# Kernel optimization log

Measured on AMD Instinct MI355X. Metric: run time of the kernel, lower is better.

Reference implementation:

```python
import jax, jax.numpy as jnp
import numpy as np

B, P, K, H, C = 8, 4096, 20, 64, 40  # clouds, points/cloud, knn k, hidden_feat, num_classes
NEG = 0.2  # LeakyReLU negative slope used by the repo MLP


def setup_inputs() -> dict:
    key = jax.random.key(0)
    ks = jax.random.split(key, 16)
    w = lambda k, shape: (jax.random.normal(k, shape, jnp.float32) / np.sqrt(shape[0]))
    return {
        "x": jax.random.normal(ks[0], (B * P, 3), jnp.float32),
        "batch": jnp.repeat(jnp.arange(B, dtype=jnp.int32), P),
        "W1": w(ks[1], (2 * 3, H)), "b1": jnp.zeros((H,), jnp.float32),
        "W2": w(ks[2], (2 * H, H)), "b2": jnp.zeros((H,), jnp.float32),
        "W3": w(ks[3], (2 * H, H)), "b3": jnp.zeros((H,), jnp.float32),
        "Wl": w(ks[4], (3 * H, 1024)), "bl": jnp.zeros((1024,), jnp.float32),
        "Wm1": w(ks[5], (1024, 256)), "bm1": jnp.zeros((256,), jnp.float32),
        "Wm2": w(ks[6], (256, 128)), "bm2": jnp.zeros((128,), jnp.float32),
        "Wo": w(ks[7], (128, C)), "bo": jnp.zeros((C,), jnp.float32),
    }


def _knn_idx(x):
    # x: [B,P,d] -> indices of K nearest neighbors (excluding self): [B,P,K]
    d2 = jnp.sum(x * x, axis=-1)  # [B,P]
    dist = d2[:, :, None] + d2[:, None, :] - 2.0 * jnp.einsum('bpd,bqd->bpq', x, x)
    dist = dist + jnp.eye(x.shape[1], dtype=x.dtype) * 1e10  # mask self-loops
    return jax.lax.top_k(-dist, K)[1]


def _edge_conv(x, W, b):
    # DynamicEdgeConv with max aggregation: nn([x_i, x_j - x_i]) maxed over K neighbors
    idx = _knn_idx(x)                                    # [B,P,K]
    x_j = jax.vmap(lambda xb, ib: xb[ib])(x, idx)        # [B,P,K,d]
    x_i = jnp.broadcast_to(x[:, :, None, :], x_j.shape)  # [B,P,K,d]
    feat = jnp.concatenate([x_i, x_j - x_i], axis=-1)    # [B,P,K,2d]
    h = jax.nn.leaky_relu(feat @ W + b, NEG)             # [B,P,K,H]
    return jnp.max(h, axis=2)                            # [B,P,H]


def reference(x, batch, W1, b1, W2, b2, W3, b3, Wl, bl, Wm1, bm1, Wm2, bm2, Wo, bo):
    # batch is sorted with equal-size clouds -> reshape to [B,P,3]
    xb = x.reshape(B, P, 3)
    x1 = _edge_conv(xb, W1, b1)
    x2 = _edge_conv(x1, W2, b2)
    x3 = _edge_conv(x2, W3, b3)
    h = jnp.concatenate([x1, x2, x3], axis=-1)           # [B,P,3H]
    h = jax.nn.leaky_relu(h @ Wl + bl, NEG)
    h = jax.nn.leaky_relu(h @ Wm1 + bm1, NEG)            # dropout = identity (eval)
    h = jax.nn.leaky_relu(h @ Wm2 + bm2, NEG)
    out = h @ Wo + bo                                    # [B,P,C]
    return jax.nn.log_softmax(out, axis=-1).reshape(B * P, C)
```

## Files before the change

kernel.cpp:

```cpp
#include <hip/hip_runtime.h>
#include <cstddef>
#include <cstdint>

constexpr int B_ = 8, P_ = 4096, K_ = 20, H_ = 64, C_ = 40;
constexpr int NPT = B_ * P_;
#define NEG_SLOPE 0.2f

typedef unsigned long long u64;
typedef unsigned int u32;
typedef unsigned short u16;
typedef __attribute__((ext_vector_type(8))) short bf16x8;
typedef __attribute__((ext_vector_type(4))) float f32x4;

__device__ inline u16 f2bf(float v) {
    u32 bits = __float_as_uint(v);
    return (u16)((bits + 0x7FFFu + ((bits >> 16) & 1)) >> 16);
}
__device__ inline float bf2f(u16 h) { return __uint_as_float((u32)h << 16); }

__device__ __forceinline__ void bubble20f(float (&a)[K_], float key) {
    float carry = key;
#pragma unroll
    for (int s = 0; s < K_; ++s) {
        float as = a[s];
        a[s]  = fminf(carry, as);
        carry = fmaxf(carry, as);
    }
}
__device__ __forceinline__ float mkkey(float dist, int cid) {
    return __uint_as_float((__float_as_uint(dist) & 0xFFFFF000u) | (u32)cid);
}

template <int D>
__global__ __launch_bounds__(256) void d2_kernel(const float* __restrict__ x,
                                                 float* __restrict__ d2) {
    int i = blockIdx.x * 256 + threadIdx.x;
    if (i >= NPT) return;
    const float* r = x + (size_t)i * D;
    float s = 0.f;
#pragma unroll
    for (int d = 0; d < D; ++d) { float v = r[d]; s += v * v; }
    d2[i] = s;
}

__global__ __launch_bounds__(256) void d2cvt3_kernel(const float* __restrict__ x,
                                                     float* __restrict__ d2,
                                                     u16* __restrict__ xh,
                                                     u16* __restrict__ xm,
                                                     u16* __restrict__ xl) {
    int i = blockIdx.x * 256 + threadIdx.x;
    if (i >= NPT) return;
    const float* r = x + (size_t)i * 64;
    float s = 0.f;
#pragma unroll
    for (int d8 = 0; d8 < 64; d8 += 8) {
        float4 v0 = *(const float4*)(r + d8);
        float4 v1 = *(const float4*)(r + d8 + 4);
        s += v0.x * v0.x + v0.y * v0.y + v0.z * v0.z + v0.w * v0.w;
        s += v1.x * v1.x + v1.y * v1.y + v1.z * v1.z + v1.w * v1.w;
        float av[8] = {v0.x, v0.y, v0.z, v0.w, v1.x, v1.y, v1.z, v1.w};
        bf16x8 vh, vm, vl;
#pragma unroll
        for (int j = 0; j < 8; ++j) {
            u16 h = f2bf(av[j]);
            float r1 = av[j] - bf2f(h);
            u16 m = f2bf(r1);
            float r2 = r1 - bf2f(m);
            vh[j] = (short)h; vm[j] = (short)m; vl[j] = (short)f2bf(r2);
        }
        *(bf16x8*)(xh + (size_t)i * 64 + d8) = vh;
        *(bf16x8*)(xm + (size_t)i * 64 + d8) = vm;
        *(bf16x8*)(xl + (size_t)i * 64 + d8) = vl;
    }
    d2[i] = s;
}

template <int D>
__global__ __launch_bounds__(256) void knnf_kernel(const float* __restrict__ x,
                                                   const float* __restrict__ d2,
                                                   int* __restrict__ idx) {
    __shared__ float sQT[D][68];
    __shared__ float sCT[D][68];
    __shared__ float sD[64][68];

    int b = blockIdx.y;
    int q0 = blockIdx.x * 64;
    const float* xc  = x + (size_t)b * P_ * D;
    const float* d2b = d2 + (size_t)b * P_;

    int t = threadIdx.x;
    int ty = t >> 4, tx = t & 15;
    int w = t >> 6, ln = t & 63;
    int qs = w * 16 + (ln >> 2);
    int cs = ln & 3;

    if (t < 64) {
#pragma unroll
        for (int d = 0; d < D; ++d) sQT[d][t] = xc[(size_t)(q0 + t) * D + d];
    }
    float qd2i[4];
#pragma unroll
    for (int i = 0; i < 4; ++i) qd2i[i] = d2b[q0 + ty * 4 + i];

    float a[K_];
#pragma unroll
    for (int s = 0; s < K_; ++s)
        a[s] = __uint_as_float(0x7F7FF000u | (u32)s);
    const float PINV = __uint_as_float(0x7F800000u);
    const float BIGF = __uint_as_float(0x7F7FFFFFu);

    float p0 = PINV, p1 = PINV, p2 = PINV, p3 = PINV;
    int pcnt = 0;
    float kthr = BIGF;

#pragma unroll 1
    for (int c0 = 0; c0 < P_; c0 += 64) {
        __syncthreads();
        if (t < 64) {
#pragma unroll
            for (int d = 0; d < D; ++d) sCT[d][t] = xc[(size_t)(c0 + t) * D + d];
        }
        __syncthreads();

        float acc[4][4] = {};
#pragma unroll
        for (int kk = 0; kk < D; ++kk) {
            float4 aq = *(const float4*)&sQT[kk][ty * 4];
            float4 bc = *(const float4*)&sCT[kk][tx * 4];
            acc[0][0] = fmaf(aq.x, bc.x, acc[0][0]); acc[0][1] = fmaf(aq.x, bc.y, acc[0][1]);
            acc[0][2] = fmaf(aq.x, bc.z, acc[0][2]); acc[0][3] = fmaf(aq.x, bc.w, acc[0][3]);
            acc[1][0] = fmaf(aq.y, bc.x, acc[1][0]); acc[1][1] = fmaf(aq.y, bc.y, acc[1][1]);
            acc[1][2] = fmaf(aq.y, bc.z, acc[1][2]); acc[1][3] = fmaf(aq.y, bc.w, acc[1][3]);
            acc[2][0] = fmaf(aq.z, bc.x, acc[2][0]); acc[2][1] = fmaf(aq.z, bc.y, acc[2][1]);
            acc[2][2] = fmaf(aq.z, bc.z, acc[2][2]); acc[2][3] = fmaf(aq.z, bc.w, acc[2][3]);
            acc[3][0] = fmaf(aq.w, bc.x, acc[3][0]); acc[3][1] = fmaf(aq.w, bc.y, acc[3][1]);
            acc[3][2] = fmaf(aq.w, bc.z, acc[3][2]); acc[3][3] = fmaf(aq.w, bc.w, acc[3][3]);
        }
        float cd2j[4];
#pragma unroll
        for (int j = 0; j < 4; ++j) cd2j[j] = d2b[c0 + tx * 4 + j];
        bool diag = (q0 == c0);
#pragma unroll
        for (int i = 0; i < 4; ++i) {
            float dd[4];
#pragma unroll
            for (int j = 0; j < 4; ++j) {
                float v = (qd2i[i] + cd2j[j]) - 2.f * acc[i][j];
                if (diag && (ty * 4 + i == tx * 4 + j)) v += 1e10f;
                dd[j] = fmaxf(v, 0.f);
            }
            *(float4*)&sD[ty * 4 + i][tx * 4] = make_float4(dd[0], dd[1], dd[2], dd[3]);
        }
        __syncthreads();

        float dvv[16];
        float mn = 3.4e38f;
#pragma unroll
        for (int u = 0; u < 16; ++u) {
            dvv[u] = sD[qs][cs + u * 4];
            mn = fminf(mn, dvv[u]);
        }
        if (__any(mn <= kthr)) {
#pragma unroll
            for (int u = 0; u < 16; ++u) {
                float dv = dvv[u];
                if (__any(dv <= kthr)) {
                    float key = mkkey(dv, c0 + cs + u * 4);
                    bool pass = key < a[K_ - 1];
                    p3 = pass ? p2 : p3;
                    p2 = pass ? p1 : p2;
                    p1 = pass ? p0 : p1;
                    p0 = pass ? key : p0;
                    pcnt = pass ? pcnt + 1 : pcnt;
                    if (__any(pcnt >= 4)) {
                        bubble20f(a, p3); bubble20f(a, p2); bubble20f(a, p1); bubble20f(a, p0);
                        p0 = p1 = p2 = p3 = PINV; pcnt = 0;
                        kthr = __uint_as_float(__float_as_uint(a[K_ - 1]) | 0xFFFu);
                    }
                }
            }
        }
    }
    bubble20f(a, p3); bubble20f(a, p2); bubble20f(a, p1); bubble20f(a, p0);

    int* op = idx + ((size_t)(b * P_ + q0 + qs)) * K_;
#pragma unroll 1
    for (int k = 0; k < K_; ++k) {
        float v = a[0];
        float v1 = __shfl_xor(v, 1);
        v = fminf(v, v1);
        float v2 = __shfl_xor(v, 2);
        v = fminf(v, v2);
        bool win = (__float_as_uint(a[0]) == __float_as_uint(v));
#pragma unroll
        for (int s = 0; s < K_ - 1; ++s) a[s] = win ? a[s + 1] : a[s];
        a[K_ - 1] = win ? BIGF : a[K_ - 1];
        if (cs == 0)
            op[k] = b * P_ + (int)(__float_as_uint(v) & 0xFFFu);
    }
}

__global__ __launch_bounds__(256) void knnm64_kernel(const u16* __restrict__ xh,
                                                     const u16* __restrict__ xm,
                                                     const u16* __restrict__ xl,
                                                     const float* __restrict__ d2,
                                                     int* __restrict__ idx) {
    __shared__ u16 sH[64 * 64];
    __shared__ u16 sM[64 * 64];
    __shared__ u16 sL[64 * 64];
    __shared__ float sd2[P_];

    int b = blockIdx.y;
    int q0 = blockIdx.x * 64;
    const u16* xhb = xh + (size_t)b * P_ * 64;
    const u16* xmb = xm + (size_t)b * P_ * 64;
    const u16* xlb = xl + (size_t)b * P_ * 64;
    const float* d2b = d2 + (size_t)b * P_;

    int t = threadIdx.x, w = t >> 6, ln = t & 63;
    int q  = ln & 15;
    int ss = ln >> 4;

    for (int i = t; i < P_ / 4; i += 256)
        ((float4*)sd2)[i] = ((const float4*)d2b)[i];

    int qrow = q0 + w * 16 + q;
    bf16x8 qh[2], qm[2], ql[2];
#pragma unroll
    for (int kt = 0; kt < 2; ++kt) {
        size_t off = (size_t)qrow * 64 + kt * 32 + ss * 8;
        qh[kt] = *(const bf16x8*)(xhb + off);
        qm[kt] = *(const bf16x8*)(xmb + off);
        ql[kt] = *(const bf16x8*)(xlb + off);
    }

    __syncthreads();
    float qd2 = sd2[qrow];

    float a[K_];
#pragma unroll
    for (int s = 0; s < K_; ++s)
        a[s] = __uint_as_float(0x7F7FF000u | (u32)s);
    const float PINV = __uint_as_float(0x7F800000u);
    const float BIGF = __uint_as_float(0x7F7FFFFFu);

    float p0 = PINV, p1 = PINV, p2 = PINV, p3 = PINV;
    int pcnt = 0;
    float kthr = BIGF;

    int sr = t >> 2;
    int sk2 = (t & 3) * 32;
    int sbase = sr * 128, sswz = (sr & 7) << 4;
    size_t sgof = (size_t)sr * 64 + (t & 3) * 16;

#pragma unroll 1
    for (int c0 = 0; c0 < P_; c0 += 64) {
        __syncthreads();
        {
            size_t g = (size_t)c0 * 64 + sgof;
            bf16x8 h0 = *(const bf16x8*)(xhb + g);
            bf16x8 h1 = *(const bf16x8*)(xhb + g + 8);
            bf16x8 m0 = *(const bf16x8*)(xmb + g);
            bf16x8 m1 = *(const bf16x8*)(xmb + g + 8);
            bf16x8 l0 = *(const bf16x8*)(xlb + g);
            bf16x8 l1 = *(const bf16x8*)(xlb + g + 8);
            *(bf16x8*)((char*)sH + sbase + (sk2 ^ sswz)) = h0;
            *(bf16x8*)((char*)sH + sbase + ((sk2 + 16) ^ sswz)) = h1;
            *(bf16x8*)((char*)sM + sbase + (sk2 ^ sswz)) = m0;
            *(bf16x8*)((char*)sM + sbase + ((sk2 + 16) ^ sswz)) = m1;
            *(bf16x8*)((char*)sL + sbase + (sk2 ^ sswz)) = l0;
            *(bf16x8*)((char*)sL + sbase + ((sk2 + 16) ^ sswz)) = l1;
        }
        __syncthreads();

        f32x4 acc[4];
#pragma unroll
        for (int nt = 0; nt < 4; ++nt) {
            acc[nt] = (f32x4){0.f, 0.f, 0.f, 0.f};
            int r = nt * 16 + q;
            int base = r * 128, swz = (r & 7) << 4;
#pragma unroll
            for (int kt = 0; kt < 2; ++kt) {
                int k2 = kt * 64 + ss * 16;
                bf16x8 ch = *(const bf16x8*)((char*)sH + base + (k2 ^ swz));
                bf16x8 cm = *(const bf16x8*)((char*)sM + base + (k2 ^ swz));
                bf16x8 cl = *(const bf16x8*)((char*)sL + base + (k2 ^ swz));
                acc[nt] = __builtin_amdgcn_mfma_f32_16x16x32_bf16(cm, qm[kt], acc[nt], 0, 0, 0);
                acc[nt] = __builtin_amdgcn_mfma_f32_16x16x32_bf16(cl, qh[kt], acc[nt], 0, 0, 0);
                acc[nt] = __builtin_amdgcn_mfma_f32_16x16x32_bf16(ch, ql[kt], acc[nt], 0, 0, 0);
                acc[nt] = __builtin_amdgcn_mfma_f32_16x16x32_bf16(cm, qh[kt], acc[nt], 0, 0, 0);
                acc[nt] = __builtin_amdgcn_mfma_f32_16x16x32_bf16(ch, qm[kt], acc[nt], 0, 0, 0);
                acc[nt] = __builtin_amdgcn_mfma_f32_16x16x32_bf16(ch, qh[kt], acc[nt], 0, 0, 0);
            }
        }

        float dvv[4][4];
        float mn = 3.4e38f;
#pragma unroll
        for (int nt = 0; nt < 4; ++nt) {
#pragma unroll
            for (int r = 0; r < 4; ++r) {
                int cID = c0 + nt * 16 + ss * 4 + r;
                float dv = (qd2 + sd2[cID]) - 2.f * acc[nt][r];
                if (cID == qrow) dv += 1e10f;
                dv = fmaxf(dv, 0.f);
                dvv[nt][r] = dv;
                mn = fminf(mn, dv);
            }
        }
        if (__any(mn <= kthr)) {
#pragma unroll
            for (int nt = 0; nt < 4; ++nt) {
#pragma unroll
                for (int r = 0; r < 4; ++r) {
                    float dv = dvv[nt][r];
                    if (__any(dv <= kthr)) {
                        float key = mkkey(dv, c0 + nt * 16 + ss * 4 + r);
                        bool pass = key < a[K_ - 1];
                        p3 = pass ? p2 : p3;
                        p2 = pass ? p1 : p2;
                        p1 = pass ? p0 : p1;
                        p0 = pass ? key : p0;
                        pcnt = pass ? pcnt + 1 : pcnt;
                        if (__any(pcnt >= 4)) {
                            bubble20f(a, p3); bubble20f(a, p2); bubble20f(a, p1); bubble20f(a, p0);
                            p0 = p1 = p2 = p3 = PINV; pcnt = 0;
                            kthr = __uint_as_float(__float_as_uint(a[K_ - 1]) | 0xFFFu);
                        }
                    }
                }
            }
        }
    }
    bubble20f(a, p3); bubble20f(a, p2); bubble20f(a, p1); bubble20f(a, p0);

    int* op = idx + ((size_t)(b * P_ + qrow)) * K_;
#pragma unroll 1
    for (int k = 0; k < K_; ++k) {
        float v = a[0];
        float v1 = __shfl_xor(v, 16);
        v = fminf(v, v1);
        float v2 = __shfl_xor(v, 32);
        v = fminf(v, v2);
        bool win = (__float_as_uint(a[0]) == __float_as_uint(v));
#pragma unroll
        for (int s = 0; s < K_ - 1; ++s) a[s] = win ? a[s + 1] : a[s];
        a[K_ - 1] = win ? BIGF : a[K_ - 1];
        if (ss == 0)
            op[k] = b * P_ + (int)(__float_as_uint(v) & 0xFFFu);
    }
}

__global__ __launch_bounds__(256) void prep_kernel(const float* __restrict__ W2,
                                                   const float* __restrict__ b2,
                                                   const float* __restrict__ W3,
                                                   const float* __restrict__ b3,
                                                   const float* __restrict__ Wl,
                                                   const float* __restrict__ Wm1,
                                                   const float* __restrict__ Wm2,
                                                   float* __restrict__ Wpk2, float* __restrict__ bpk2,
                                                   float* __restrict__ Wpk3, float* __restrict__ bpk3,
                                                   u16* __restrict__ WlT,
                                                   u16* __restrict__ Wm1T,
                                                   u16* __restrict__ Wm2T) {
    int t = blockIdx.x * 256 + threadIdx.x;
    if (t < 8192) {
        int d = t >> 7, h2 = t & 127;
        Wpk2[t] = (h2 < 64) ? W2[d * 64 + h2] : W2[(64 + d) * 64 + (h2 - 64)];
        if (t < 128) bpk2[t] = (t < 64) ? b2[t] : 0.f;
    } else if (t < 16384) {
        int t2 = t - 8192;
        int d = t2 >> 7, h2 = t2 & 127;
        Wpk3[t2] = (h2 < 64) ? W3[d * 64 + h2] : W3[(64 + d) * 64 + (h2 - 64)];
        if (t2 < 128) bpk3[t2] = (t2 < 64) ? b3[t2] : 0.f;
    } else if (t < 212992) {
        int t2 = t - 16384;
        int k = t2 >> 10, n = t2 & 1023;
        WlT[(size_t)n * 192 + k] = f2bf(Wl[t2]);
    } else if (t < 475136) {
        int t2 = t - 212992;
        int k = t2 >> 8, n = t2 & 255;
        Wm1T[(size_t)n * 1024 + k] = f2bf(Wm1[t2]);
    } else if (t < 507904) {
        int t2 = t - 475136;
        int k = t2 >> 7, n = t2 & 127;
        Wm2T[(size_t)n * 256 + k] = f2bf(Wm2[t2]);
    }
}

__global__ __launch_bounds__(256) void uv3_kernel(const float* __restrict__ x,
                                                  const float* __restrict__ W,
                                                  const float* __restrict__ b,
                                                  float* __restrict__ UV) {
    int t = blockIdx.x * 256 + threadIdx.x;
    int p = t >> 7, h2 = t & 127;
    float x0 = x[p * 3], x1 = x[p * 3 + 1], x2 = x[p * 3 + 2];
    float r;
    if (h2 < 64) {
        r = b[h2] + x0 * W[h2] + x1 * W[64 + h2] + x2 * W[128 + h2];
    } else {
        int h = h2 - 64;
        r = x0 * W[192 + h] + x1 * W[256 + h] + x2 * W[320 + h];
    }
    UV[t] = r;
}

__global__ __launch_bounds__(256) void edgemax_kernel(const float* __restrict__ UV,
                                                      const int* __restrict__ idx,
                                                      float* __restrict__ xout) {
    int wv = threadIdx.x >> 6, lane = threadIdx.x & 63;
    int p = blockIdx.x * 4 + wv;
    const float* uvp = UV + (size_t)p * 128;
    float duv = uvp[lane] - uvp[64 + lane];
    const int* ip = idx + (size_t)p * K_;
    int jj[K_];
#pragma unroll
    for (int k = 0; k < K_; ++k) jj[k] = ip[k];
    float m = -3.4e38f;
#pragma unroll
    for (int k = 0; k < K_; ++k) {
        float vj = UV[(size_t)jj[k] * 128 + 64 + lane];
        float t = duv + vj;
        m = fmaxf(m, fmaxf(t, NEG_SLOPE * t));
    }
    xout[(size_t)p * H_ + lane] = m;
}

__global__ __launch_bounds__(256) void gemm_kernel(const float* __restrict__ A1,
                                                   const float* __restrict__ Wm,
                                                   const float* __restrict__ bias,
                                                   float* __restrict__ Cm,
                                                   int M, int N, int Kd, int leaky) {
    __shared__ float sA[32][68];
    __shared__ float sB[32][68];

    int tid = threadIdx.x;
    int row0 = blockIdx.x * 64, col0 = blockIdx.y * 64;
    int tx = tid & 15, ty = tid >> 4;

    int lr  = tid >> 2;
    int lk4 = (tid & 3) * 4;
    int lkb = tid >> 4;
    int lnb = (tid & 15) * 4;

    float acc[4][4] = {};

    for (int k0 = 0; k0 < Kd; k0 += 32) {
        int arow = row0 + lr;
#pragma unroll
        for (int h = 0; h < 32; h += 16) {
            int kk = k0 + lk4 + h;
            const float* src = A1 + (size_t)arow * Kd + kk;
            float4 av = *(const float4*)src;
            sA[lk4 + h + 0][lr] = av.x; sA[lk4 + h + 1][lr] = av.y;
            sA[lk4 + h + 2][lr] = av.z; sA[lk4 + h + 3][lr] = av.w;
        }
        int bcol = col0 + lnb;
#pragma unroll
        for (int h = 0; h < 32; h += 16) {
            float4 bv = make_float4(0.f, 0.f, 0.f, 0.f);
            if (bcol < N) bv = *(const float4*)(Wm + (size_t)(k0 + lkb + h) * N + bcol);
            *(float4*)&sB[lkb + h][lnb] = bv;
        }
        __syncthreads();

#pragma unroll
        for (int kk2 = 0; kk2 < 32; ++kk2) {
            float4 a = *(const float4*)&sA[kk2][ty * 4];
            float4 bb = *(const float4*)&sB[kk2][tx * 4];
            acc[0][0] = fmaf(a.x, bb.x, acc[0][0]); acc[0][1] = fmaf(a.x, bb.y, acc[0][1]);
            acc[0][2] = fmaf(a.x, bb.z, acc[0][2]); acc[0][3] = fmaf(a.x, bb.w, acc[0][3]);
            acc[1][0] = fmaf(a.y, bb.x, acc[1][0]); acc[1][1] = fmaf(a.y, bb.y, acc[1][1]);
            acc[1][2] = fmaf(a.y, bb.z, acc[1][2]); acc[1][3] = fmaf(a.y, bb.w, acc[1][3]);
            acc[2][0] = fmaf(a.z, bb.x, acc[2][0]); acc[2][1] = fmaf(a.z, bb.y, acc[2][1]);
            acc[2][2] = fmaf(a.z, bb.z, acc[2][2]); acc[2][3] = fmaf(a.z, bb.w, acc[2][3]);
            acc[3][0] = fmaf(a.w, bb.x, acc[3][0]); acc[3][1] = fmaf(a.w, bb.y, acc[3][1]);
            acc[3][2] = fmaf(a.w, bb.z, acc[3][2]); acc[3][3] = fmaf(a.w, bb.w, acc[3][3]);
        }
        __syncthreads();
    }

    for (int i = 0; i < 4; ++i) {
        int row = row0 + ty * 4 + i;
        for (int j = 0; j < 4; ++j) {
            int col = col0 + tx * 4 + j;
            if (col < N) {
                float v = acc[i][j] + bias[col];
                if (leaky) v = v > 0.f ? v : NEG_SLOPE * v;
                Cm[(size_t)row * N + col] = v;
            }
        }
    }
}

template <int KD, int OUT_BF16>
__global__ __launch_bounds__(256) void gemm_mfma_kernel(const u16* __restrict__ A,
                                                        const u16* __restrict__ BT,
                                                        const float* __restrict__ bias,
                                                        void* __restrict__ Cout,
                                                        int N, int leaky) {
    __shared__ u16 sA[128 * 64];
    __shared__ u16 sB[128 * 64];

    int t = threadIdx.x;
    int wave = t >> 6, lane = t & 63;
    int wm = wave >> 1, wn = wave & 1;
    int row0 = blockIdx.x * 128;
    int col0 = blockIdx.y * 128;

    f32x4 acc[4][4] = {};

    for (int k0 = 0; k0 < KD; k0 += 64) {
        __syncthreads();
#pragma unroll
        for (int i = 0; i < 4; ++i) {
            int li = t + i * 256;
            int r = li >> 3;
            int kc = (li & 7) * 8;
            bf16x8 v = *(const bf16x8*)(A + (size_t)(row0 + r) * KD + k0 + kc);
            *(bf16x8*)((char*)sA + r * 128 + ((kc * 2) ^ ((r & 7) << 4))) = v;
        }
#pragma unroll
        for (int i = 0; i < 4; ++i) {
            int li = t + i * 256;
            int n = li >> 3;
            int kc = (li & 7) * 8;
            bf16x8 v = *(const bf16x8*)(BT + (size_t)(col0 + n) * KD + k0 + kc);
            *(bf16x8*)((char*)sB + n * 128 + ((kc * 2) ^ ((n & 7) << 4))) = v;
        }
        __syncthreads();

#pragma unroll
        for (int kk = 0; kk < 2; ++kk) {
            int kb = kk * 64 + (lane >> 4) * 16;
            bf16x8 af[4], bfr[4];
#pragma unroll
            for (int mi = 0; mi < 4; ++mi) {
                int r = wm * 64 + mi * 16 + (lane & 15);
                af[mi] = *(const bf16x8*)((char*)sA + r * 128 + (kb ^ ((r & 7) << 4)));
            }
#pragma unroll
            for (int ni = 0; ni < 4; ++ni) {
                int n = wn * 64 + ni * 16 + (lane & 15);
                bfr[ni] = *(const bf16x8*)((char*)sB + n * 128 + (kb ^ ((n & 7) << 4)));
            }
#pragma unroll
            for (int mi = 0; mi < 4; ++mi)
#pragma unroll
                for (int ni = 0; ni < 4; ++ni)
                    acc[mi][ni] = __builtin_amdgcn_mfma_f32_16x16x32_bf16(
                        af[mi], bfr[ni], acc[mi][ni], 0, 0, 0);
        }
    }

#pragma unroll
    for (int ni = 0; ni < 4; ++ni) {
        int col = col0 + wn * 64 + ni * 16 + (lane & 15);
        float bs = bias[col];
#pragma unroll
        for (int mi = 0; mi < 4; ++mi) {
#pragma unroll
            for (int r = 0; r < 4; ++r) {
                int row = row0 + wm * 64 + mi * 16 + (lane >> 4) * 4 + r;
                float v = acc[mi][ni][r] + bs;
                if (leaky) v = v > 0.f ? v : NEG_SLOPE * v;
                if (OUT_BF16)
                    ((u16*)Cout)[(size_t)row * N + col] = f2bf(v);
                else
                    ((float*)Cout)[(size_t)row * N + col] = v;
            }
        }
    }
}

__global__ __launch_bounds__(256) void gemm_mfma_cat_kernel(const float* __restrict__ x1,
                                                            const float* __restrict__ x2,
                                                            const float* __restrict__ x3,
                                                            const u16* __restrict__ BT,
                                                            const float* __restrict__ bias,
                                                            u16* __restrict__ Cout,
                                                            int N) {
    __shared__ u16 sA[128 * 64];
    __shared__ u16 sB[128 * 64];

    int t = threadIdx.x;
    int wave = t >> 6, lane = t & 63;
    int wm = wave >> 1, wn = wave & 1;
    int row0 = blockIdx.x * 128;
    int col0 = blockIdx.y * 128;

    f32x4 acc[4][4] = {};

#pragma unroll 1
    for (int k0 = 0; k0 < 192; k0 += 64) {
        const float* src = (k0 == 0) ? x1 : (k0 == 64) ? x2 : x3;
        __syncthreads();
#pragma unroll
        for (int i = 0; i < 4; ++i) {
            int li = t + i * 256;
            int r = li >> 3;
            int kc = (li & 7) * 8;
            const float* sp = src + (size_t)(row0 + r) * 64 + kc;
            float4 a0 = *(const float4*)sp;
            float4 a1 = *(const float4*)(sp + 4);
            bf16x8 v;
            v[0] = (short)f2bf(a0.x); v[1] = (short)f2bf(a0.y);
            v[2] = (short)f2bf(a0.z); v[3] = (short)f2bf(a0.w);
            v[4] = (short)f2bf(a1.x); v[5] = (short)f2bf(a1.y);
            v[6] = (short)f2bf(a1.z); v[7] = (short)f2bf(a1.w);
            *(bf16x8*)((char*)sA + r * 128 + ((kc * 2) ^ ((r & 7) << 4))) = v;
        }
#pragma unroll
        for (int i = 0; i < 4; ++i) {
            int li = t + i * 256;
            int n = li >> 3;
            int kc = (li & 7) * 8;
            bf16x8 v = *(const bf16x8*)(BT + (size_t)(col0 + n) * 192 + k0 + kc);
            *(bf16x8*)((char*)sB + n * 128 + ((kc * 2) ^ ((n & 7) << 4))) = v;
        }
        __syncthreads();

#pragma unroll
        for (int kk = 0; kk < 2; ++kk) {
            int kb = kk * 64 + (lane >> 4) * 16;
            bf16x8 af[4], bfr[4];
#pragma unroll
            for (int mi = 0; mi < 4; ++mi) {
                int r = wm * 64 + mi * 16 + (lane & 15);
                af[mi] = *(const bf16x8*)((char*)sA + r * 128 + (kb ^ ((r & 7) << 4)));
            }
#pragma unroll
            for (int ni = 0; ni < 4; ++ni) {
                int n = wn * 64 + ni * 16 + (lane & 15);
                bfr[ni] = *(const bf16x8*)((char*)sB + n * 128 + (kb ^ ((n & 7) << 4)));
            }
#pragma unroll
            for (int mi = 0; mi < 4; ++mi)
#pragma unroll
                for (int ni = 0; ni < 4; ++ni)
                    acc[mi][ni] = __builtin_amdgcn_mfma_f32_16x16x32_bf16(
                        af[mi], bfr[ni], acc[mi][ni], 0, 0, 0);
        }
    }

#pragma unroll
    for (int ni = 0; ni < 4; ++ni) {
        int col = col0 + wn * 64 + ni * 16 + (lane & 15);
        float bs = bias[col];
#pragma unroll
        for (int mi = 0; mi < 4; ++mi) {
#pragma unroll
            for (int r = 0; r < 4; ++r) {
                int row = row0 + wm * 64 + mi * 16 + (lane >> 4) * 4 + r;
                float v = acc[mi][ni][r] + bs;
                v = v > 0.f ? v : NEG_SLOPE * v;
                Cout[(size_t)row * N + col] = f2bf(v);
            }
        }
    }
}

__global__ __launch_bounds__(256) void lsm_wo_kernel(const float* __restrict__ act3,
                                                     const float* __restrict__ Wo,
                                                     const float* __restrict__ bo,
                                                     float* __restrict__ out) {
    __shared__ float sWo[128 * 44];
    __shared__ float sAct[4][128];

    int t = threadIdx.x;
    for (int i = t; i < 128 * 40; i += 256) {
        int k = i / 40, c = i % 40;
        sWo[k * 44 + c] = Wo[i];
    }
    __syncthreads();

    int wv = t >> 6, lane = t & 63;
    int row = blockIdx.x * 4 + wv;
    sAct[wv][lane]      = act3[(size_t)row * 128 + lane];
    sAct[wv][64 + lane] = act3[(size_t)row * 128 + 64 + lane];

    float acc = (lane < C_) ? bo[lane] : -3.4e38f;
    if (lane < C_) {
#pragma unroll 8
        for (int k = 0; k < 128; ++k)
            acc = fmaf(sAct[wv][k], sWo[k * 44 + lane], acc);
    }
    float m = acc;
#pragma unroll
    for (int s = 1; s < 64; s <<= 1) m = fmaxf(m, __shfl_xor(m, s));
    float e = (lane < C_) ? expf(acc - m) : 0.f;
    float sum = e;
#pragma unroll
    for (int s = 1; s < 64; s <<= 1) sum += __shfl_xor(sum, s);
    if (lane < C_) out[(size_t)row * C_ + lane] = acc - m - logf(sum);
}

extern "C" void kernel_launch(void* const* d_in, const int* in_sizes, int n_in,
                              void* d_out, int out_size, void* d_ws, size_t ws_size,
                              hipStream_t stream) {
    const float* x   = (const float*)d_in[0];
    const float* W1  = (const float*)d_in[2];
    const float* b1  = (const float*)d_in[3];
    const float* W2  = (const float*)d_in[4];
    const float* b2  = (const float*)d_in[5];
    const float* W3  = (const float*)d_in[6];
    const float* b3  = (const float*)d_in[7];
    const float* Wl  = (const float*)d_in[8];
    const float* bl  = (const float*)d_in[9];
    const float* Wm1 = (const float*)d_in[10];
    const float* bm1 = (const float*)d_in[11];
    const float* Wm2 = (const float*)d_in[12];
    const float* bm2 = (const float*)d_in[13];
    const float* Wo  = (const float*)d_in[14];
    const float* bo  = (const float*)d_in[15];
    float* out = (float*)d_out;

    char* ws = (char*)d_ws;
    float* x1   = (float*)(ws);
    float* x2   = (float*)(ws + 8388608);
    float* x3   = (float*)(ws + 16777216);
    int*   idx  = (int*)  (ws + 25165824);
    float* d2   = (float*)(ws + 27787264);
    char* hb = ws + 27918336;
    u16*   xhs  = (u16*)(hb);
    u16*   xms  = (u16*)(hb + 4194304);
    u16*   xls  = (u16*)(hb + 8388608);
    float* UV   = (float*)(hb);
    float* Wpk2 = (float*)(ws + 44695552);
    float* bpk2 = (float*)(ws + 44728320);
    float* Wpk3 = (float*)(ws + 44728832);
    float* bpk3 = (float*)(ws + 44761600);
    u16*   WlT  = (u16*)  (ws + 44762112);
    u16*   Wm1T = (u16*)  (ws + 45155328);
    u16*   Wm2T = (u16*)  (ws + 45679616);
    u16*   act1 = (u16*)(hb);
    u16*   act2 = (u16*)(ws + 45745152);
    float* act3 = (float*)(hb);

    prep_kernel<<<1984, 256, 0, stream>>>(W2, b2, W3, b3, Wl, Wm1, Wm2,
                                          Wpk2, bpk2, Wpk3, bpk3, WlT, Wm1T, Wm2T);

    d2_kernel<3><<<NPT / 256, 256, 0, stream>>>(x, d2);
    knnf_kernel<3><<<dim3(P_ / 64, B_), 256, 0, stream>>>(x, d2, idx);
    uv3_kernel<<<NPT * 128 / 256, 256, 0, stream>>>(x, W1, b1, UV);
    edgemax_kernel<<<NPT / 4, 256, 0, stream>>>(UV, idx, x1);
    d2cvt3_kernel<<<NPT / 256, 256, 0, stream>>>(x1, d2, xhs, xms, xls);
    knnm64_kernel<<<dim3(P_ / 64, B_), 256, 0, stream>>>(xhs, xms, xls, d2, idx);
    gemm_kernel<<<dim3(NPT / 64, 2), 256, 0, stream>>>(x1, Wpk2, bpk2, UV, NPT, 128, 64, 0);
    edgemax_kernel<<<NPT / 4, 256, 0, stream>>>(UV, idx, x2);
    d2cvt3_kernel<<<NPT / 256, 256, 0, stream>>>(x2, d2, xhs, xms, xls);
    knnm64_kernel<<<dim3(P_ / 64, B_), 256, 0, stream>>>(xhs, xms, xls, d2, idx);
    gemm_kernel<<<dim3(NPT / 64, 2), 256, 0, stream>>>(x2, Wpk3, bpk3, UV, NPT, 128, 64, 0);
    edgemax_kernel<<<NPT / 4, 256, 0, stream>>>(UV, idx, x3);

    for (int c = 0; c < 4; ++c) {
        size_t r0 = (size_t)c * 8192;
        gemm_mfma_cat_kernel<<<dim3(64, 8), 256, 0, stream>>>(x1 + r0 * 64, x2 + r0 * 64,
                                                              x3 + r0 * 64, WlT, bl, act1, 1024);
        gemm_mfma_kernel<1024, 1><<<dim3(64, 2), 256, 0, stream>>>(act1, Wm1T, bm1, act2, 256, 1);
        gemm_mfma_kernel<256, 0><<<dim3(64, 1), 256, 0, stream>>>(act2, Wm2T, bm2, act3, 128, 1);
        lsm_wo_kernel<<<2048, 256, 0, stream>>>(act3, Wo, bo, out + r0 * C_);
    }
}
```

Before: 942.2 us.

## Drop third bf16 split in 64-d kNN and rewrite 3-d kNN as per-lane scan

The 64-dim kNN distance GEMM now splits inputs into two bf16 parts (hi, mid) instead of three, cutting MFMAs per tile from six to three and removing the low-part buffer, its shared tile and its global loads. Separately, the 3-d kNN kernel drops its shared-memory tiled FMA GEMM and staged distance matrix: each lane computes distances directly from a small shared candidate array holding xyz plus the squared norm, and the final merge uses lane shuffles across 16 and 32. The precision cut lowers dot-product accuracy to roughly 16 mantissa bits, which could change near-tie neighbour choices compared with the fp32 reference.

```diff
diff --git a/kernel.cpp b/kernel.cpp
--- a/kernel.cpp
+++ b/kernel.cpp
@@ -43,11 +43,10 @@
     d2[i] = s;
 }
 
-__global__ __launch_bounds__(256) void d2cvt3_kernel(const float* __restrict__ x,
+__global__ __launch_bounds__(256) void d2cvt2_kernel(const float* __restrict__ x,
                                                      float* __restrict__ d2,
                                                      u16* __restrict__ xh,
-                                                     u16* __restrict__ xm,
-                                                     u16* __restrict__ xl) {
+                                                     u16* __restrict__ xm) {
     int i = blockIdx.x * 256 + threadIdx.x;
     if (i >= NPT) return;
     const float* r = x + (size_t)i * 64;
@@ -59,48 +58,38 @@
         s += v0.x * v0.x + v0.y * v0.y + v0.z * v0.z + v0.w * v0.w;
         s += v1.x * v1.x + v1.y * v1.y + v1.z * v1.z + v1.w * v1.w;
         float av[8] = {v0.x, v0.y, v0.z, v0.w, v1.x, v1.y, v1.z, v1.w};
-        bf16x8 vh, vm, vl;
+        bf16x8 vh, vm;
 #pragma unroll
         for (int j = 0; j < 8; ++j) {
             u16 h = f2bf(av[j]);
             float r1 = av[j] - bf2f(h);
-            u16 m = f2bf(r1);
-            float r2 = r1 - bf2f(m);
-            vh[j] = (short)h; vm[j] = (short)m; vl[j] = (short)f2bf(r2);
+            vh[j] = (short)h; vm[j] = (short)f2bf(r1);
         }
         *(bf16x8*)(xh + (size_t)i * 64 + d8) = vh;
         *(bf16x8*)(xm + (size_t)i * 64 + d8) = vm;
-        *(bf16x8*)(xl + (size_t)i * 64 + d8) = vl;
     }
     d2[i] = s;
 }
 
-template <int D>
-__global__ __launch_bounds__(256) void knnf_kernel(const float* __restrict__ x,
-                                                   const float* __restrict__ d2,
-                                                   int* __restrict__ idx) {
-    __shared__ float sQT[D][68];
-    __shared__ float sCT[D][68];
-    __shared__ float sD[64][68];
+__global__ __launch_bounds__(256) void knnf3_kernel(const float* __restrict__ x,
+                                                    const float* __restrict__ d2,
+                                                    int* __restrict__ idx) {
+    __shared__ float sC[64][4];
 
     int b = blockIdx.y;
     int q0 = blockIdx.x * 64;
-    const float* xc  = x + (size_t)b * P_ * D;
+    const float* xc  = x + (size_t)b * P_ * 3;
     const float* d2b = d2 + (size_t)b * P_;
 
-    int t = threadIdx.x;
-    int ty = t >> 4, tx = t & 15;
-    int w = t >> 6, ln = t & 63;
-    int qs = w * 16 + (ln >> 2);
-    int cs = ln & 3;
-
-    if (t < 64) {
-#pragma unroll
-        for (int d = 0; d < D; ++d) sQT[d][t] = xc[(size_t)(q0 + t) * D + d];
-    }
-    float qd2i[4];
-#pragma unroll
-    for (int i = 0; i < 4; ++i) qd2i[i] = d2b[q0 + ty * 4 + i];
+    int t = threadIdx.x, w = t >> 6, ln = t & 63;
+    int q  = ln & 15;
+    int ss = ln >> 4;
+
+    int qrow = q0 + w * 16 + q;
+    float qx = xc[(size_t)qrow * 3];
+    float qy = xc[(size_t)qrow * 3 + 1];
+    float qz = xc[(size_t)qrow * 3 + 2];
+    float qd2 = d2b[qrow];
 
     float a[K_];
 #pragma unroll
@@ -113,59 +102,26 @@
     int pcnt = 0;
     float kthr = BIGF;
 
+    int scc = t >> 2, scm = t & 3;
+
 #pragma unroll 1
     for (int c0 = 0; c0 < P_; c0 += 64) {
         __syncthreads();
-        if (t < 64) {
-#pragma unroll
-            for (int d = 0; d < D; ++d) sCT[d][t] = xc[(size_t)(c0 + t) * D + d];
-        }
-        __syncthreads();
-
-        float acc[4][4] = {};
-#pragma unroll
-        for (int kk = 0; kk < D; ++kk) {
-            float4 aq = *(const float4*)&sQT[kk][ty * 4];
-            float4 bc = *(const float4*)&sCT[kk][tx * 4];
-            acc[0][0] = fmaf(aq.x, bc.x, acc[0][0]); acc[0][1] = fmaf(aq.x, bc.y, acc[0][1]);
-            acc[0][2] = fmaf(aq.x, bc.z, acc[0][2]); acc[0][3] = fmaf(aq.x, bc.w, acc[0][3]);
-            acc[1][0] = fmaf(aq.y, bc.x, acc[1][0]); acc[1][1] = fmaf(aq.y, bc.y, acc[1][1]);
-            acc[1][2] = fmaf(aq.y, bc.z, acc[1][2]); acc[1][3] = fmaf(aq.y, bc.w, acc[1][3]);
-            acc[2][0] = fmaf(aq.z, bc.x, acc[2][0]); acc[2][1] = fmaf(aq.z, bc.y, acc[2][1]);
-            acc[2][2] = fmaf(aq.z, bc.z, acc[2][2]); acc[2][3] = fmaf(aq.z, bc.w, acc[2][3]);
-            acc[3][0] = fmaf(aq.w, bc.x, acc[3][0]); acc[3][1] = fmaf(aq.w, bc.y, acc[3][1]);
-            acc[3][2] = fmaf(aq.w, bc.z, acc[3][2]); acc[3][3] = fmaf(aq.w, bc.w, acc[3][3]);
-        }
-        float cd2j[4];
-#pragma unroll
-        for (int j = 0; j < 4; ++j) cd2j[j] = d2b[c0 + tx * 4 + j];
-        bool diag = (q0 == c0);
-#pragma unroll
-        for (int i = 0; i < 4; ++i) {
-            float dd[4];
-#pragma unroll
-            for (int j = 0; j < 4; ++j) {
-                float v = (qd2i[i] + cd2j[j]) - 2.f * acc[i][j];
-                if (diag && (ty * 4 + i == tx * 4 + j)) v += 1e10f;
-                dd[j] = fmaxf(v, 0.f);
-            }
-            *(float4*)&sD[ty * 4 + i][tx * 4] = make_float4(dd[0], dd[1], dd[2], dd[3]);
-        }
-        __syncthreads();
-
-        float dvv[16];
-        float mn = 3.4e38f;
-#pragma unroll
-        for (int u = 0; u < 16; ++u) {
-            dvv[u] = sD[qs][cs + u * 4];
-            mn = fminf(mn, dvv[u]);
-        }
-        if (__any(mn <= kthr)) {
-#pragma unroll
-            for (int u = 0; u < 16; ++u) {
-                float dv = dvv[u];
+        sC[scc][scm] = (scm < 3) ? xc[(size_t)(c0 + scc) * 3 + scm] : d2b[c0 + scc];
+        __syncthreads();
+
+#pragma unroll
+        for (int nt = 0; nt < 4; ++nt) {
+#pragma unroll
+            for (int r = 0; r < 4; ++r) {
+                int cl = nt * 16 + ss * 4 + r;
+                int cID = c0 + cl;
+                float4 cv = *(const float4*)&sC[cl][0];
+                float dv = (qd2 + cv.w) - 2.f * (qx * cv.x + qy * cv.y + qz * cv.z);
+                if (cID == qrow) dv += 1e10f;
+                dv = fmaxf(dv, 0.f);
                 if (__any(dv <= kthr)) {
-                    float key = mkkey(dv, c0 + cs + u * 4);
+                    float key = mkkey(dv, cID);
                     bool pass = key < a[K_ - 1];
                     p3 = pass ? p2 : p3;
                     p2 = pass ? p1 : p2;
@@ -183,38 +139,35 @@
     }
     bubble20f(a, p3); bubble20f(a, p2); bubble20f(a, p1); bubble20f(a, p0);
 
-    int* op = idx + ((size_t)(b * P_ + q0 + qs)) * K_;
+    int* op = idx + ((size_t)(b * P_ + qrow)) * K_;
 #pragma unroll 1
     for (int k = 0; k < K_; ++k) {
         float v = a[0];
-        float v1 = __shfl_xor(v, 1);
+        float v1 = __shfl_xor(v, 16);
         v = fminf(v, v1);
-        float v2 = __shfl_xor(v, 2);
+        float v2 = __shfl_xor(v, 32);
         v = fminf(v, v2);
         bool win = (__float_as_uint(a[0]) == __float_as_uint(v));
 #pragma unroll
         for (int s = 0; s < K_ - 1; ++s) a[s] = win ? a[s + 1] : a[s];
         a[K_ - 1] = win ? BIGF : a[K_ - 1];
-        if (cs == 0)
+        if (ss == 0)
             op[k] = b * P_ + (int)(__float_as_uint(v) & 0xFFFu);
     }
 }
 
 __global__ __launch_bounds__(256) void knnm64_kernel(const u16* __restrict__ xh,
                                                      const u16* __restrict__ xm,
-                                                     const u16* __restrict__ xl,
                                                      const float* __restrict__ d2,
                                                      int* __restrict__ idx) {
     __shared__ u16 sH[64 * 64];
     __shared__ u16 sM[64 * 64];
-    __shared__ u16 sL[64 * 64];
     __shared__ float sd2[P_];
 
     int b = blockIdx.y;
     int q0 = blockIdx.x * 64;
     const u16* xhb = xh + (size_t)b * P_ * 64;
     const u16* xmb = xm + (size_t)b * P_ * 64;
-    const u16* xlb = xl + (size_t)b * P_ * 64;
     const float* d2b = d2 + (size_t)b * P_;
 
     int t = threadIdx.x, w = t >> 6, ln = t & 63;
@@ -225,13 +178,12 @@
         ((float4*)sd2)[i] = ((const float4*)d2b)[i];
 
     int qrow = q0 + w * 16 + q;
-    bf16x8 qh[2], qm[2], ql[2];
+    bf16x8 qh[2], qm[2];
 #pragma unroll
     for (int kt = 0; kt < 2; ++kt) {
         size_t off = (size_t)qrow * 64 + kt * 32 + ss * 8;
         qh[kt] = *(const bf16x8*)(xhb + off);
         qm[kt] = *(const bf16x8*)(xmb + off);
-        ql[kt] = *(const bf16x8*)(xlb + off);
     }
 
     __syncthreads();
@@ -262,14 +214,10 @@
             bf16x8 h1 = *(const bf16x8*)(xhb + g + 8);
             bf16x8 m0 = *(const bf16x8*)(xmb + g);
             bf16x8 m1 = *(const bf16x8*)(xmb + g + 8);
-            bf16x8 l0 = *(const bf16x8*)(xlb + g);
-            bf16x8 l1 = *(const bf16x8*)(xlb + g + 8);
             *(bf16x8*)((char*)sH + sbase + (sk2 ^ sswz)) = h0;
             *(bf16x8*)((char*)sH + sbase + ((sk2 + 16) ^ sswz)) = h1;
             *(bf16x8*)((char*)sM + sbase + (sk2 ^ sswz)) = m0;
             *(bf16x8*)((char*)sM + sbase + ((sk2 + 16) ^ sswz)) = m1;
-            *(bf16x8*)((char*)sL + sbase + (sk2 ^ sswz)) = l0;
-            *(bf16x8*)((char*)sL + sbase + ((sk2 + 16) ^ sswz)) = l1;
         }
         __syncthreads();
 
@@ -284,10 +232,6 @@
                 int k2 = kt * 64 + ss * 16;
                 bf16x8 ch = *(const bf16x8*)((char*)sH + base + (k2 ^ swz));
                 bf16x8 cm = *(const bf16x8*)((char*)sM + base + (k2 ^ swz));
-                bf16x8 cl = *(const bf16x8*)((char*)sL + base + (k2 ^ swz));
-                acc[nt] = __builtin_amdgcn_mfma_f32_16x16x32_bf16(cm, qm[kt], acc[nt], 0, 0, 0);
-                acc[nt] = __builtin_amdgcn_mfma_f32_16x16x32_bf16(cl, qh[kt], acc[nt], 0, 0, 0);
-                acc[nt] = __builtin_amdgcn_mfma_f32_16x16x32_bf16(ch, ql[kt], acc[nt], 0, 0, 0);
                 acc[nt] = __builtin_amdgcn_mfma_f32_16x16x32_bf16(cm, qh[kt], acc[nt], 0, 0, 0);
                 acc[nt] = __builtin_amdgcn_mfma_f32_16x16x32_bf16(ch, qm[kt], acc[nt], 0, 0, 0);
                 acc[nt] = __builtin_amdgcn_mfma_f32_16x16x32_bf16(ch, qh[kt], acc[nt], 0, 0, 0);
@@ -724,7 +668,6 @@
     char* hb = ws + 27918336;
     u16*   xhs  = (u16*)(hb);
     u16*   xms  = (u16*)(hb + 4194304);
-    u16*   xls  = (u16*)(hb + 8388608);
     float* UV   = (float*)(hb);
     float* Wpk2 = (float*)(ws + 44695552);
     float* bpk2 = (float*)(ws + 44728320);
@@ -741,15 +684,15 @@
                                           Wpk2, bpk2, Wpk3, bpk3, WlT, Wm1T, Wm2T);
 
     d2_kernel<3><<<NPT / 256, 256, 0, stream>>>(x, d2);
-    knnf_kernel<3><<<dim3(P_ / 64, B_), 256, 0, stream>>>(x, d2, idx);
+    knnf3_kernel<<<dim3(P_ / 64, B_), 256, 0, stream>>>(x, d2, idx);
     uv3_kernel<<<NPT * 128 / 256, 256, 0, stream>>>(x, W1, b1, UV);
     edgemax_kernel<<<NPT / 4, 256, 0, stream>>>(UV, idx, x1);
-    d2cvt3_kernel<<<NPT / 256, 256, 0, stream>>>(x1, d2, xhs, xms, xls);
-    knnm64_kernel<<<dim3(P_ / 64, B_), 256, 0, stream>>>(xhs, xms, xls, d2, idx);
+    d2cvt2_kernel<<<NPT / 256, 256, 0, stream>>>(x1, d2, xhs, xms);
+    knnm64_kernel<<<dim3(P_ / 64, B_), 256, 0, stream>>>(xhs, xms, d2, idx);
     gemm_kernel<<<dim3(NPT / 64, 2), 256, 0, stream>>>(x1, Wpk2, bpk2, UV, NPT, 128, 64, 0);
     edgemax_kernel<<<NPT / 4, 256, 0, stream>>>(UV, idx, x2);
-    d2cvt3_kernel<<<NPT / 256, 256, 0, stream>>>(x2, d2, xhs, xms, xls);
-    knnm64_kernel<<<dim3(P_ / 64, B_), 256, 0, stream>>>(xhs, xms, xls, d2, idx);
+    d2cvt2_kernel<<<NPT / 256, 256, 0, stream>>>(x2, d2, xhs, xms);
+    knnm64_kernel<<<dim3(P_ / 64, B_), 256, 0, stream>>>(xhs, xms, d2, idx);
     gemm_kernel<<<dim3(NPT / 64, 2), 256, 0, stream>>>(x2, Wpk3, bpk3, UV, NPT, 128, 64, 0);
     edgemax_kernel<<<NPT / 4, 256, 0, stream>>>(UV, idx, x3);
 
```

Result: faster. 897.5 us (-4.7%).
